# Kernel optimization log

Measured on AMD Instinct MI355X. Metric: run time of the kernel, lower is better.

The kernel has to match this reference:

```python
import jax, jax.numpy as jnp
import numpy as np

BS = 16
CIN = 32          # input_channels
COUT = 64         # out_channels
OUT_DIM = 1024    # out_dim
S = 2
S0 = 1
K = S * (S0 + 1)  # non-overlapping patch size = 4
D = OUT_DIM * K   # input spatial length = 4096


def setup_inputs() -> dict:
    key = jax.random.key(0)
    k1, k2 = jax.random.split(key)
    x = jax.random.normal(k1, (BS, CIN, D), dtype=jnp.float32)
    # learned parameter, torch.randn init
    weight = jax.random.normal(k2, (COUT, CIN, D), dtype=jnp.float32)
    return {"x": x, "weight": weight}


def reference(x, weight):
    # sharing == 0 path of NonOverlappingLocallyConnected1d:
    #   out[b,o,p] = (1/sqrt(CIN)) * sum_{c,k} x[b,c,p*K+k] * weight[o,c,p*K+k]
    # Original materializes [bs,cout,cin,D] via broadcast multiply then sums
    # over (cin, K); fused here as a single einsum over non-overlapping patches.
    bs = x.shape[0]
    xr = x.reshape(bs, CIN, OUT_DIM, K)        # [b, c, p, k]
    wr = weight.reshape(COUT, CIN, OUT_DIM, K)  # [o, c, p, k]
    out = jnp.einsum('bcpk,ocpk->bop', xr, wr)  # [b, o, p]
    return out / jnp.sqrt(jnp.asarray(CIN, x.dtype))
```

## Files before the change

kernel.cpp:

```cpp
#include <hip/hip_runtime.h>

#define BS      16
#define CIN     32
#define COUT    64
#define OUT_DIM 1024
#define DD      4096

#define OT      4
#define PT      64
#define CCH     8
#define NCH     (CIN / CCH)

__global__ __launch_bounds__(512, 2) void nolc1d_kernel(
    const float* __restrict__ x,
    const float* __restrict__ w,
    float* __restrict__ out)
{
    const int bid = blockIdx.x;
    const int xcd = bid & 7;
    const int j   = bid >> 3;
    const int og  = j & 15;
    const int pg  = xcd + 8 * (j >> 4);
    const int o0  = og * OT;
    const int p0  = pg * PT;

    const int t    = threadIdx.x;
    const int lane = t & 63;
    const int wv   = t >> 6;
    const int b0   = wv * 2;

    __shared__ float4 ws4[2][CCH * OT * 64];

    const float4* __restrict__ x4 = (const float4*)x;
    const float4* __restrict__ w4 = (const float4*)w;
    const int rs = DD / 4;

    auto stage = [&](int buf, int ch) {
        #pragma unroll
        for (int i = 0; i < 4; ++i) {
            const int r    = wv * 4 + i;
            const int c_in = r >> 2;
            const int o_in = r & 3;
            const int c    = ch * CCH + c_in;
            ws4[buf][r * 64 + lane] =
                w4[((size_t)(o0 + o_in) * CIN + c) * rs + p0 + lane];
        }
    };

    float acc[2][OT] = {};

    stage(0, 0);
    __syncthreads();

    for (int ch = 0; ch < NCH; ++ch) {
        if (ch + 1 < NCH) stage((ch + 1) & 1, ch + 1);
        const int buf = ch & 1;

        #pragma unroll
        for (int ci = 0; ci < CCH; ++ci) {
            const int c = ch * CCH + ci;
            const float4 xv0 = x4[((size_t)b0       * CIN + c) * rs + p0 + lane];
            const float4 xv1 = x4[((size_t)(b0 + 1) * CIN + c) * rs + p0 + lane];
            #pragma unroll
            for (int o = 0; o < OT; ++o) {
                const float4 wvv = ws4[buf][(ci * OT + o) * 64 + lane];
                acc[0][o] += xv0.x * wvv.x + xv0.y * wvv.y +
                             xv0.z * wvv.z + xv0.w * wvv.w;
                acc[1][o] += xv1.x * wvv.x + xv1.y * wvv.y +
                             xv1.z * wvv.z + xv1.w * wvv.w;
            }
        }
        __syncthreads();
    }

    const float scale = 0.17677669529663687f;
    #pragma unroll
    for (int bi = 0; bi < 2; ++bi) {
        #pragma unroll
        for (int o = 0; o < OT; ++o) {
            out[((size_t)(b0 + bi) * COUT + (o0 + o)) * OUT_DIM + p0 + lane] =
                acc[bi][o] * scale;
        }
    }
}

extern "C" void kernel_launch(void* const* d_in, const int* in_sizes, int n_in,
                              void* d_out, int out_size, void* d_ws, size_t ws_size,
                              hipStream_t stream) {
    const float* x = (const float*)d_in[0];
    const float* w = (const float*)d_in[1];
    float* out = (float*)d_out;

    nolc1d_kernel<<<dim3(256), dim3(512), 0, stream>>>(x, w, out);
}
```

Before: 90.58 us.

## Retile to 8 outputs x 4 batches per thread with cross-wave channel-split reduction

```diff
diff --git a/kernel.cpp b/kernel.cpp
--- a/kernel.cpp
+++ b/kernel.cpp
@@ -4,12 +4,10 @@
 #define CIN     32
 #define COUT    64
 #define OUT_DIM 1024
-#define DD      4096
+#define RS4     1024
 
-#define OT      4
-#define PT      64
-#define CCH     8
-#define NCH     (CIN / CCH)
+#define OT      8
+#define PT      32
 
 __global__ __launch_bounds__(512, 2) void nolc1d_kernel(
     const float* __restrict__ x,
@@ -18,69 +16,93 @@
 {
     const int bid = blockIdx.x;
     const int xcd = bid & 7;
-    const int j   = bid >> 3;
-    const int og  = j & 15;
-    const int pg  = xcd + 8 * (j >> 4);
+    const int r   = bid >> 3;
+    const int og  = r & 7;
+    const int pg  = xcd + 8 * (r >> 3);
     const int o0  = og * OT;
-    const int p0  = pg * PT;
+    const int pf0 = pg * PT;
 
     const int t    = threadIdx.x;
     const int lane = t & 63;
     const int wv   = t >> 6;
-    const int b0   = wv * 2;
+    const int g    = wv & 3;
+    const int cs   = ((wv >> 2) << 1) | (lane >> 5);
+    const int pp   = lane & 31;
 
-    __shared__ float4 ws4[2][CCH * OT * 64];
+    __shared__ float4 ws4[2][2048];
 
     const float4* __restrict__ x4 = (const float4*)x;
     const float4* __restrict__ w4 = (const float4*)w;
-    const int rs = DD / 4;
 
     auto stage = [&](int buf, int ch) {
         #pragma unroll
         for (int i = 0; i < 4; ++i) {
-            const int r    = wv * 4 + i;
-            const int c_in = r >> 2;
-            const int o_in = r & 3;
-            const int c    = ch * CCH + c_in;
-            ws4[buf][r * 64 + lane] =
-                w4[((size_t)(o0 + o_in) * CIN + c) * rs + p0 + lane];
+            const int L  = t + 512 * i;
+            const int cl = L >> 8;
+            const int o  = (L >> 5) & 7;
+            const int q  = L & 31;
+            ws4[buf][L] =
+                w4[((o0 + o) * CIN + (ch * 8 + cl)) * RS4 + pf0 + q];
         }
     };
 
-    float acc[2][OT] = {};
+    float acc[4][OT] = {};
+    const int xb = (4 * g * CIN + cs) * RS4 + pf0 + pp;
 
     stage(0, 0);
     __syncthreads();
 
-    for (int ch = 0; ch < NCH; ++ch) {
-        if (ch + 1 < NCH) stage((ch + 1) & 1, ch + 1);
+    #pragma unroll
+    for (int ch = 0; ch < 4; ++ch) {
+        if (ch < 3) stage((ch + 1) & 1, ch + 1);
         const int buf = ch & 1;
-
         #pragma unroll
-        for (int ci = 0; ci < CCH; ++ci) {
-            const int c = ch * CCH + ci;
-            const float4 xv0 = x4[((size_t)b0       * CIN + c) * rs + p0 + lane];
-            const float4 xv1 = x4[((size_t)(b0 + 1) * CIN + c) * rs + p0 + lane];
+        for (int j = 0; j < 2; ++j) {
+            const int c8 = 2 * ch + j;
+            float4 xv[4];
+            #pragma unroll
+            for (int bi = 0; bi < 4; ++bi)
+                xv[bi] = x4[xb + bi * (CIN * RS4) + c8 * 4 * RS4];
+            const int cl = cs + 4 * j;
             #pragma unroll
             for (int o = 0; o < OT; ++o) {
-                const float4 wvv = ws4[buf][(ci * OT + o) * 64 + lane];
-                acc[0][o] += xv0.x * wvv.x + xv0.y * wvv.y +
-                             xv0.z * wvv.z + xv0.w * wvv.w;
-                acc[1][o] += xv1.x * wvv.x + xv1.y * wvv.y +
-                             xv1.z * wvv.z + xv1.w * wvv.w;
+                const float4 wq = ws4[buf][(cl * 8 + o) * 32 + pp];
+                #pragma unroll
+                for (int bi = 0; bi < 4; ++bi)
+                    acc[bi][o] += xv[bi].x * wq.x + xv[bi].y * wq.y +
+                                  xv[bi].z * wq.z + xv[bi].w * wq.w;
             }
         }
         __syncthreads();
     }
 
+    float4* red = &ws4[0][0];
+    #pragma unroll
+    for (int o = 0; o < OT; ++o)
+        red[cs * 1024 + (g * 8 + o) * 32 + pp] =
+            make_float4(acc[0][o], acc[1][o], acc[2][o], acc[3][o]);
+    __syncthreads();
+
     const float scale = 0.17677669529663687f;
     #pragma unroll
-    for (int bi = 0; bi < 2; ++bi) {
-        #pragma unroll
-        for (int o = 0; o < OT; ++o) {
-            out[((size_t)(b0 + bi) * COUT + (o0 + o)) * OUT_DIM + p0 + lane] =
-                acc[bi][o] * scale;
-        }
+    for (int jj = 0; jj < 2; ++jj) {
+        const int idx = t + 512 * jj;
+        const int g2  = idx >> 8;
+        const int oo  = (idx >> 5) & 7;
+        const int p2  = idx & 31;
+        const float4 a = red[idx];
+        const float4 b = red[idx + 1024];
+        const float4 c = red[idx + 2048];
+        const float4 d = red[idx + 3072];
+        const int p = pf0 + p2;
+        out[((4 * g2 + 0) * COUT + o0 + oo) * OUT_DIM + p] =
+            (a.x + b.x + c.x + d.x) * scale;
+        out[((4 * g2 + 1) * COUT + o0 + oo) * OUT_DIM + p] =
+            (a.y + b.y + c.y + d.y) * scale;
+        out[((4 * g2 + 2) * COUT + o0 + oo) * OUT_DIM + p] =
+            (a.z + b.z + c.z + d.z) * scale;
+        out[((4 * g2 + 3) * COUT + o0 + oo) * OUT_DIM + p] =
+            (a.w + b.w + c.w + d.w) * scale;
     }
 }
 
```

Measured after the change: 120.3 us. +32.9%, slower.
